# Performance work log

Hardware: AMD Instinct MI355X
Metric: run time of the kernel (lower is better)

## Reference

```python
import math
import jax, jax.numpy as jnp
import numpy as np

_INIT_LOG_GAIN = math.log(5.0)
B, L, D = 4, 1024, 256


def setup_inputs() -> dict:
    key = jax.random.key(0)
    kq, kk = jax.random.split(key)
    q = jax.random.normal(kq, (B, L, D), dtype=jnp.float32)
    k = jax.random.normal(kk, (B, L, D), dtype=jnp.float32)
    P_prev = jnp.zeros((B, D, D), dtype=jnp.float32)
    log_gain = jnp.full((D,), _INIT_LOG_GAIN, dtype=jnp.float32)
    output_scale = jnp.ones((D,), dtype=jnp.float32)
    return {"q": q, "k": k, "P_prev": P_prev, "log_gain": log_gain,
            "output_scale": output_scale}


def reference(q, k, P_prev, log_gain, output_scale):
    """Sequential rank-1 projection-state update + normalized matvec + gated tanh.

    q, k: [B, L, D]; P_prev: [B, D, D]. Returns (q_out [B,L,D], P_final [B,D,D]).
    """
    gain = jnp.exp(log_gain)  # effective gain, [D]

    def step(P, qk_t):
        q_t, k_t = qk_t                                   # each [B, D]
        P = P + jnp.einsum('bi,bj->bij', k_t, k_t)        # rank-1 update
        fro = jnp.sqrt(jnp.sum(P * P, axis=(-2, -1), keepdims=True))
        P_norm = P / (fro + 1e-7)
        q_aligned = jnp.einsum('bij,bj->bi', P_norm, q_t)
        q_safe = jnp.tanh(gain * q_aligned) * output_scale
        return P, q_safe

    # scan over the L time axis
    P_final, outs = jax.lax.scan(step, P_prev,
                                 (jnp.swapaxes(q, 0, 1), jnp.swapaxes(k, 0, 1)))
    q_out = jnp.swapaxes(outs, 0, 1)  # [B, L, D]
    return q_out, P_final
```

## Files before the change

### kernel.cpp

```cpp
#include <hip/hip_runtime.h>
#include <math.h>


typedef __attribute__((ext_vector_type(8))) short bf16x8;
typedef __attribute__((ext_vector_type(4))) float f32x4;

__device__ __forceinline__ unsigned short f2bf(float x) {
    union { float f; unsigned u; } c; c.f = x;
    return (unsigned short)((c.u + (0x7fffu + ((c.u >> 16) & 1u))) >> 16);
}
__device__ __forceinline__ unsigned f2bf2(float a, float b) {
    union { float f; unsigned u; } ca, cb; ca.f = a; cb.f = b;
    unsigned ua = ca.u + (0x7fffu + ((ca.u >> 16) & 1u));
    unsigned ub = cb.u + (0x7fffu + ((cb.u >> 16) & 1u));
    return (ua >> 16) | (ub & 0xffff0000u);
}
__device__ __forceinline__ float bf2f(unsigned short h) {
    union { unsigned u; float f; } c; c.u = ((unsigned)h) << 16; return c.f;
}
__device__ __forceinline__ void gload16(const void* g, const void* l) {
    __builtin_amdgcn_global_load_lds(
        (const __attribute__((address_space(1))) unsigned int*)g,
        (__attribute__((address_space(3))) unsigned int*)l, 16, 0, 0);
}
__device__ __forceinline__ bf16x8 ldsfrag(const unsigned short* lds, int row0, int g0, int lane) {
    int r = row0 + (lane & 15);
    int g = g0 + (lane >> 4);
    return *(const bf16x8*)(lds + r * 64 + (((g ^ (r & 7)) & 7) << 3));
}
#define MFMA16(a, b, c) __builtin_amdgcn_mfma_f32_16x16x32_bf16(a, b, c, 0, 0, 0)

__global__ __launch_bounds__(256) void k_prep(
    const float* __restrict__ Q, const float* __restrict__ K,
    const float* __restrict__ Pprev,
    unsigned short* __restrict__ Qb, unsigned short* __restrict__ Kb,
    unsigned short* __restrict__ KThi, unsigned short* __restrict__ KTlo,
    float* __restrict__ basePart, int B_, int L, int D)
{
    __shared__ float lds[64 * 65];
    int tid = threadIdx.x, lane = tid & 63, w = tid >> 6;
    int nDt = D >> 6, nLt = L >> 6;
    int nC = B_ * nLt * nDt;
    int id = blockIdx.x;
    if (id < nC) {
        int dt = id % nDt, lt = (id / nDt) % nLt, b = id / (nDt * nLt);
        int l0 = lt * 64, d0 = dt * 64;
        const float* Qf = Q + (size_t)b * L * D;
        const float* Kf = K + (size_t)b * L * D;
        unsigned short* Qbp = Qb + (size_t)b * L * D;
        unsigned short* Kbp = Kb + (size_t)b * L * D;
        unsigned short* KThp = KThi + (size_t)b * D * L;
        unsigned short* KTlp = KTlo + (size_t)b * D * L;
        int r = tid >> 2, cq = (tid & 3) << 4;
#pragma unroll
        for (int i = 0; i < 16; i += 4) {
            float4 qv = *(const float4*)(Qf + (size_t)(l0 + r) * D + d0 + cq + i);
            float4 kv = *(const float4*)(Kf + (size_t)(l0 + r) * D + d0 + cq + i);
            uint2 qo; qo.x = f2bf2(qv.x, qv.y); qo.y = f2bf2(qv.z, qv.w);
            uint2 ko; ko.x = f2bf2(kv.x, kv.y); ko.y = f2bf2(kv.z, kv.w);
            *(uint2*)(Qbp + (size_t)(l0 + r) * D + d0 + cq + i) = qo;
            *(uint2*)(Kbp + (size_t)(l0 + r) * D + d0 + cq + i) = ko;
            lds[r * 65 + cq + i]     = kv.x; lds[r * 65 + cq + i + 1] = kv.y;
            lds[r * 65 + cq + i + 2] = kv.z; lds[r * 65 + cq + i + 3] = kv.w;
        }
        __syncthreads();
        int d2 = tid >> 2, cl = (tid & 3) << 4;
#pragma unroll
        for (int i = 0; i < 16; i += 2) {
            float v0 = lds[(cl + i) * 65 + d2];
            float v1 = lds[(cl + i + 1) * 65 + d2];
            unsigned short h0 = f2bf(v0), h1 = f2bf(v1);
            size_t off = (size_t)(d0 + d2) * L + l0 + cl + i;
            *(unsigned*)(KThp + off) = (unsigned)h0 | ((unsigned)h1 << 16);
            *(unsigned*)(KTlp + off) = f2bf2(v0 - bf2f(h0), v1 - bf2f(h1));
        }
    } else {
        int id2 = id - nC;
        int n = D * D / 16;
        const float* P = Pprev + (size_t)(id2 >> 4) * D * D + (size_t)(id2 & 15) * n;
        float s = 0.f;
        for (int i = tid * 4; i < n; i += 1024) {
            float4 vv = *(const float4*)(P + i);
            s += vv.x * vv.x + vv.y * vv.y + vv.z * vv.z + vv.w * vv.w;
        }
#pragma unroll
        for (int off = 32; off; off >>= 1) s += __shfl_down(s, off);
        if (lane == 0) lds[w] = s;
        __syncthreads();
        if (tid == 0) basePart[id2] = lds[0] + lds[1] + lds[2] + lds[3];
    }
}

__global__ __launch_bounds__(256) void k_gs(
    const unsigned short* __restrict__ Qb, const unsigned short* __restrict__ Kb,
    unsigned short* __restrict__ Sc, float* __restrict__ r2d,
    int B_, int L, int D, int nT, int nPairs)
{
    __shared__ unsigned short smem[24576];
    int tid = threadIdx.x, lane = tid & 63, w = tid >> 6;
    int fr = lane & 15, fq = lane >> 4;
    int nGS = B_ * nPairs;
    int bx = blockIdx.x;
    int id = (bx & 7) * (nGS >> 3) + (bx >> 3);

    int p = id % nPairs;
    int b = id / nPairs;
    int ti = (int)((sqrtf(8.f * p + 1.f) - 1.f) * 0.5f);
    while ((ti + 1) * (ti + 2) / 2 <= p) ti++;
    while (ti * (ti + 1) / 2 > p) ti--;
    int sj = p - ti * (ti + 1) / 2;

    const unsigned short* Qp = Qb + (size_t)b * L * D;
    const unsigned short* Kp = Kb + (size_t)b * L * D;
    int t0 = ti * 64, s0 = sj * 64;
    int wr = w >> 1, wc = w & 1;

    f32x4 g00 = {0,0,0,0}, g01 = {0,0,0,0}, g10 = {0,0,0,0}, g11 = {0,0,0,0};
    f32x4 s00 = {0,0,0,0}, s01 = {0,0,0,0}, s10 = {0,0,0,0}, s11 = {0,0,0,0};

    auto STAGE = [&](int ck, int bo) {
        const unsigned short* Kt = Kp + (size_t)t0 * D + ck * 64;
        const unsigned short* Qt = Qp + (size_t)t0 * D + ck * 64;
        const unsigned short* Ks = Kp + (size_t)s0 * D + ck * 64;
        for (int c = w; c < 8; c += 4) {
            int lrow = c * 8 + (lane >> 3);
            int gof = lrow * D + ((((lane & 7) ^ (lrow & 7)) & 7) << 3);
            gload16(Kt + gof, smem + bo + c * 512);
            gload16(Qt + gof, smem + bo + 4096 + c * 512);
            gload16(Ks + gof, smem + bo + 8192 + c * 512);
        }
    };

    STAGE(0, 0);
    __syncthreads();
    for (int ck = 0; ck < 4; ck++) {
        int cur = (ck & 1) * 12288;
        if (ck < 3) STAGE(ck + 1, 12288 - cur);
        const unsigned short* Kt = smem + cur;
        const unsigned short* Qt = Kt + 4096;
        const unsigned short* Ks = Kt + 8192;
#pragma unroll
        for (int kc = 0; kc < 2; kc++) {
            bf16x8 bK0 = ldsfrag(Ks, wc * 32, kc * 4, lane);
            bf16x8 bK1 = ldsfrag(Ks, wc * 32 + 16, kc * 4, lane);
            bf16x8 aK0 = ldsfrag(Kt, wr * 32, kc * 4, lane);
            bf16x8 aK1 = ldsfrag(Kt, wr * 32 + 16, kc * 4, lane);
            bf16x8 aQ0 = ldsfrag(Qt, wr * 32, kc * 4, lane);
            bf16x8 aQ1 = ldsfrag(Qt, wr * 32 + 16, kc * 4, lane);
            g00 = MFMA16(aK0, bK0, g00);
            g01 = MFMA16(aK0, bK1, g01);
            g10 = MFMA16(aK1, bK0, g10);
            g11 = MFMA16(aK1, bK1, g11);
            s00 = MFMA16(aQ0, bK0, s00);
            s01 = MFMA16(aQ0, bK1, s01);
            s10 = MFMA16(aQ1, bK0, s10);
            s11 = MFMA16(aQ1, bK1, s11);
        }
        __syncthreads();
    }

    float rsv[2][4] = {{0, 0, 0, 0}, {0, 0, 0, 0}};
#define EPI(MI, NI, AG, AS) { _Pragma("unroll") \
    for (int reg = 0; reg < 4; reg++) { \
        int tl = wr * 32 + MI * 16 + fq * 4 + reg; \
        int sl2 = wc * 32 + NI * 16 + fr; \
        int t = ti * 64 + tl, s = sj * 64 + sl2; \
        float g = AG[reg]; \
        float wgt = (s < t) ? 2.f : (s == t ? 1.f : 0.f); \
        rsv[MI][reg] += wgt * g * g; \
        smem[tl * 64 + sl2] = f2bf((s <= t) ? AS[reg] : 0.f); \
    } }
    EPI(0, 0, g00, s00) EPI(0, 1, g01, s01)
    EPI(1, 0, g10, s10) EPI(1, 1, g11, s11)
#undef EPI
    __syncthreads();
    {
        unsigned short* ScT = Sc + ((size_t)(b * nPairs + p) << 12);
        const uint4* s4 = (const uint4*)smem;
        uint4* d4 = (uint4*)ScT;
        d4[tid] = s4[tid];
        d4[tid + 256] = s4[tid + 256];
    }
#pragma unroll
    for (int off = 1; off < 16; off <<= 1) {
#pragma unroll
        for (int mi = 0; mi < 2; mi++)
#pragma unroll
            for (int reg = 0; reg < 4; reg++)
                rsv[mi][reg] += __shfl_xor(rsv[mi][reg], off);
    }
    if (fr == 0) {
#pragma unroll
        for (int mi = 0; mi < 2; mi++)
#pragma unroll
            for (int reg = 0; reg < 4; reg++) {
                int t = ti * 64 + wr * 32 + mi * 16 + fq * 4 + reg;
                r2d[((size_t)(b * 2 * nT) + sj * 2 + wc) * L + t] = rsv[mi][reg];
            }
    }
}

__global__ __launch_bounds__(256) void k_scan(
    const float* __restrict__ K, const float* __restrict__ Pprev,
    const float* __restrict__ r2d, const float* __restrict__ basePart,
    float* __restrict__ invfro, int B_, int L, int D, int nT)
{
    __shared__ float wred[4];
    int b = blockIdx.x;
    int tid = threadIdx.x, lane = tid & 63, w = tid >> 6;
    float bb = 0.f;
#pragma unroll
    for (int i = 0; i < 16; i++) bb += basePart[b * 16 + i];

    int t0v = tid * 4;
    int ns = 2 * ((t0v >> 6) + 1);
    float4 vs = {0.f, 0.f, 0.f, 0.f};
    for (int j = 0; j < ns; j++) {
        float4 rr = *(const float4*)&r2d[((size_t)(b * 2 * nT) + j) * L + t0v];
        vs.x += rr.x; vs.y += rr.y; vs.z += rr.z; vs.w += rr.w;
    }
    float v[4] = {vs.x, vs.y, vs.z, vs.w};
    if (bb != 0.f) {
#pragma unroll
        for (int u2 = 0; u2 < 4; u2++) {
            int t = t0v + u2;
            const float* kt = K + ((size_t)b * L + t) * D;
            const float* P = Pprev + (size_t)b * D * D;
            float c = 0.f;
            for (int i = 0; i < D; i++) {
                float a2 = 0.f;
                for (int j2 = 0; j2 < D; j2++) a2 += P[i * D + j2] * kt[j2];
                c += kt[i] * a2;
            }
            v[u2] += 2.f * c;
        }
    }
    v[1] += v[0]; v[2] += v[1]; v[3] += v[2];
    float tot = v[3], sc2 = tot;
    for (int off = 1; off < 64; off <<= 1) {
        float n2 = __shfl_up(sc2, off);
        if (lane >= off) sc2 += n2;
    }
    if (lane == 63) wred[w] = sc2;
    __syncthreads();
    float woff = 0.f;
    for (int i2 = 0; i2 < w; i2++) woff += wred[i2];
    float exc = woff + sc2 - tot;
#pragma unroll
    for (int u2 = 0; u2 < 4; u2++)
        invfro[(size_t)b * L + t0v + u2] = 1.f / (sqrtf(bb + exc + v[u2]) + 1e-7f);
}

__global__ __launch_bounds__(256) void k_yp(
    const float* __restrict__ Q,
    const float* __restrict__ Pprev, const float* __restrict__ log_gain,
    const float* __restrict__ oscale,
    const unsigned short* __restrict__ Sc, const float* __restrict__ invfro,
    const unsigned short* __restrict__ KThi, const unsigned short* __restrict__ KTlo,
    const float* __restrict__ basePart,
    float* __restrict__ out, float* __restrict__ outP,
    int B_, int L, int D, int nT, int nPairs)
{
    __shared__ unsigned short ys[18432];
    __shared__ float invf[1024];
    int tid = threadIdx.x, lane = tid & 63, w = tid >> 6;
    int fr = lane & 15, fq = lane >> 4;
    int nDh = 16;
    int nY = B_ * (nT >> 1) * nDh;
    int bx = blockIdx.x;
    int id = (bx < nY) ? ((bx & 7) * (nY >> 3) + (bx >> 3)) : bx;

    if (id < nY) {
        int dh = id % nDh;
        int u = (id / nDh) % (nT >> 1);
        int b = id / (nDh * (nT >> 1));
        int d0 = dh * 16;

        float bb = 0.f;
#pragma unroll
        for (int i = 0; i < 16; i++) bb += basePart[b * 16 + i];
        *(float4*)&invf[tid * 4] = *(const float4*)&invfro[(size_t)b * L + tid * 4];
        __syncthreads();

        int twl = w << 4;
        int ti0 = u, ti1 = nT - 1 - u;
        int pb0 = ti0 * (ti0 + 1) / 2, pb1 = ti1 * (ti1 + 1) / 2;
        const unsigned short* ScB = Sc + ((size_t)b * nPairs << 12);
        const unsigned short* KTb = KThi + (size_t)b * D * L;

        f32x4 c0 = {0, 0, 0, 0};
        f32x4 c1 = {0, 0, 0, 0};

        auto STAGE = [&](int sj, int bo) {
            const unsigned short* T1p = ScB + ((size_t)(pb1 + sj) << 12);
            if (sj <= u) {
                const unsigned short* T0p = ScB + ((size_t)(pb0 + sj) << 12);
                for (int c = w; c < 8; c += 4) {
                    int lrow = c * 8 + (lane >> 3);
                    int go = lrow * 64 + ((((lane & 7) ^ (lrow & 7)) & 7) << 3);
                    gload16(T0p + go, ys + bo + c * 512);
                }
            }
            for (int c = w; c < 8; c += 4) {
                int lrow = c * 8 + (lane >> 3);
                int go = lrow * 64 + ((((lane & 7) ^ (lrow & 7)) & 7) << 3);
                gload16(T1p + go, ys + bo + 4096 + c * 512);
            }
            if (w < 2) {
                int lrow = w * 8 + (lane >> 3);
                int gsw = (((lane & 7) ^ (lrow & 7)) & 7) << 3;
                gload16(KTb + (size_t)(d0 + lrow) * L + sj * 64 + gsw,
                        ys + bo + 8192 + w * 512);
            }
        };

        STAGE(0, 0);
        __syncthreads();
        for (int sj = 0; sj <= ti1; sj++) {
            int cur = (sj & 1) * 9216;
            if (sj < ti1) STAGE(sj + 1, 9216 - cur);
            const unsigned short* S0 = ys + cur;
            const unsigned short* S1 = S0 + 4096;
            const unsigned short* KTl = S0 + 8192;
#pragma unroll
            for (int kc = 0; kc < 2; kc++) {
                bf16x8 b0 = ldsfrag(KTl, 0, kc * 4, lane);
                bf16x8 A1 = ldsfrag(S1, twl, kc * 4, lane);
                c1 = MFMA16(A1, b0, c1);
                if (sj <= ti0) {
                    bf16x8 A0 = ldsfrag(S0, twl, kc * 4, lane);
                    c0 = MFMA16(A0, b0, c0);
                }
            }
            __syncthreads();
        }

        if (bb != 0.f) {
            const float* Qf = Q + (size_t)b * L * D;
            const float* Pb = Pprev + (size_t)b * D * D;
            for (int jj = 0; jj < D; jj++) {
                float p0 = Pb[(size_t)(d0 + fr) * D + jj];
#pragma unroll
                for (int reg = 0; reg < 4; reg++) {
                    float q0v = Qf[(size_t)(ti0 * 64 + twl + fq * 4 + reg) * D + jj];
                    float q1v = Qf[(size_t)(ti1 * 64 + twl + fq * 4 + reg) * D + jj];
                    c0[reg] += q0v * p0;
                    c1[reg] += q1v * p0;
                }
            }
        }

        float gg0 = expf(log_gain[d0 + fr]), os0 = oscale[d0 + fr];
        float* outb = out + (size_t)b * L * D;
#pragma unroll
        for (int reg = 0; reg < 4; reg++) {
            int t0 = ti0 * 64 + twl + fq * 4 + reg;
            int t1 = ti1 * 64 + twl + fq * 4 + reg;
            outb[(size_t)t0 * D + d0 + fr] = tanhf(gg0 * c0[reg] * invf[t0]) * os0;
            outb[(size_t)t1 * D + d0 + fr] = tanhf(gg0 * c1[reg] * invf[t1]) * os0;
        }
    } else {
        int id2 = id - nY;
        int b = id2 >> 4, ij = id2 & 15;
        int i0 = (ij >> 2) << 6, j0 = (ij & 3) << 6;
        const unsigned short* Hb = KThi + (size_t)b * D * L;
        const unsigned short* Lb = KTlo + (size_t)b * D * L;
        int wr = w >> 1, wc = w & 1;
        unsigned short* Ah = ys;
        unsigned short* Al = ys + 4096;
        unsigned short* Bh = ys + 8192;
        unsigned short* Bl = ys + 12288;

        f32x4 c00 = {0,0,0,0}, c01 = {0,0,0,0}, c10 = {0,0,0,0}, c11 = {0,0,0,0};
        for (int ck = 0; ck < 16; ck++) {
            __syncthreads();
            for (int c = w; c < 8; c += 4) {
                int lrow = c * 8 + (lane >> 3);
                int gof = (((lane & 7) ^ (lrow & 7)) & 7) << 3;
                gload16(Hb + (size_t)(i0 + lrow) * L + ck * 64 + gof, Ah + c * 512);
                gload16(Lb + (size_t)(i0 + lrow) * L + ck * 64 + gof, Al + c * 512);
                gload16(Hb + (size_t)(j0 + lrow) * L + ck * 64 + gof, Bh + c * 512);
                gload16(Lb + (size_t)(j0 + lrow) * L + ck * 64 + gof, Bl + c * 512);
            }
            __syncthreads();
#pragma unroll
            for (int kc = 0; kc < 2; kc++) {
                bf16x8 ah0 = ldsfrag(Ah, wr * 32, kc * 4, lane);
                bf16x8 ah1 = ldsfrag(Ah, wr * 32 + 16, kc * 4, lane);
                bf16x8 al0 = ldsfrag(Al, wr * 32, kc * 4, lane);
                bf16x8 al1 = ldsfrag(Al, wr * 32 + 16, kc * 4, lane);
                bf16x8 bh0 = ldsfrag(Bh, wc * 32, kc * 4, lane);
                bf16x8 bh1 = ldsfrag(Bh, wc * 32 + 16, kc * 4, lane);
                bf16x8 bl0 = ldsfrag(Bl, wc * 32, kc * 4, lane);
                bf16x8 bl1 = ldsfrag(Bl, wc * 32 + 16, kc * 4, lane);
                c00 = MFMA16(ah0, bh0, c00); c00 = MFMA16(ah0, bl0, c00); c00 = MFMA16(al0, bh0, c00);
                c01 = MFMA16(ah0, bh1, c01); c01 = MFMA16(ah0, bl1, c01); c01 = MFMA16(al0, bh1, c01);
                c10 = MFMA16(ah1, bh0, c10); c10 = MFMA16(ah1, bl0, c10); c10 = MFMA16(al1, bh0, c10);
                c11 = MFMA16(ah1, bh1, c11); c11 = MFMA16(ah1, bl1, c11); c11 = MFMA16(al1, bh1, c11);
            }
        }
        const float* Pb = Pprev + (size_t)b * D * D;
        float* Ob = outP + (size_t)b * D * D;
#define PEPI(MI, NI, ACC) { _Pragma("unroll") \
        for (int reg = 0; reg < 4; reg++) { \
            int i = i0 + wr * 32 + MI * 16 + fq * 4 + reg; \
            int j = j0 + wc * 32 + NI * 16 + fr; \
            Ob[(size_t)i * D + j] = Pb[(size_t)i * D + j] + ACC[reg]; \
        } }
        PEPI(0, 0, c00) PEPI(0, 1, c01) PEPI(1, 0, c10) PEPI(1, 1, c11)
#undef PEPI
    }
}

extern "C" void kernel_launch(void* const* d_in, const int* in_sizes, int n_in,
                              void* d_out, int out_size, void* d_ws, size_t ws_size,
                              hipStream_t stream) {
    const float* q = (const float*)d_in[0];
    const float* k = (const float*)d_in[1];
    const float* Pprev = (const float*)d_in[2];
    const float* log_gain = (const float*)d_in[3];
    const float* oscale = (const float*)d_in[4];

    int D = in_sizes[3];
    int B = in_sizes[2] / (D * D);
    int L = in_sizes[0] / (B * D);
    int nT = L / 64;
    int nPairs = nT * (nT + 1) / 2;
    int nDt = D >> 6;
    int nLt = L >> 6;

    if (D != 256 || L != 1024) return;

    float* out = (float*)d_out;
    float* outP = out + (size_t)B * L * D;

    size_t sR = (size_t)B * L * 2 * nT;
    size_t sBP = 64;
    size_t sI = (size_t)B * L;
    size_t sSc = (size_t)B * nPairs * 4096;
    size_t sLD = (size_t)B * L * D;
    size_t sKT = (size_t)B * D * L;
    size_t need = (sR + sBP + sI) * sizeof(float) + (sSc + 2 * sLD + 2 * sKT) * 2;
    if (ws_size < need) return;

    float* r2d = (float*)d_ws;
    float* basePart = r2d + sR;
    float* invfro = basePart + sBP;
    unsigned short* Sc = (unsigned short*)(invfro + sI);
    unsigned short* Qb = Sc + sSc;
    unsigned short* Kb = Qb + sLD;
    unsigned short* KThi = Kb + sLD;
    unsigned short* KTlo = KThi + sKT;

    int grid0 = B * nLt * nDt + B * 16;
    int grid1 = B * nPairs;
    int grid2 = B * (nT >> 1) * 16 + B * nDt * nDt;

    k_prep<<<grid0, 256, 0, stream>>>(q, k, Pprev, Qb, Kb, KThi, KTlo, basePart, B, L, D);
    k_gs<<<grid1, 256, 0, stream>>>(Qb, Kb, Sc, r2d, B, L, D, nT, nPairs);
    k_scan<<<B, 256, 0, stream>>>(k, Pprev, r2d, basePart, invfro, B, L, D, nT);
    k_yp<<<grid2, 256, 0, stream>>>(q, Pprev, log_gain, oscale, Sc, invfro, KThi, KTlo,
                                    basePart, out, outP, B, L, D, nT, nPairs);
}
```

Measured before the change: 48.86 us.

## Fold norm scan into output kernel and move P-final GEMM into Gram kernel

Removes the separate single-block-per-batch k_scan launch. Each output block now recomputes the Frobenius-norm prefix scan into shared memory from r2d, so the invfro workspace goes away. The P_final update blocks move from the output kernel into the Gram/score kernel's grid so they run alongside it. This cuts one launch and its serialization bubble, at the cost of every k_y block redundantly redoing the small 1024-element scan.

```diff
diff --git a/kernel.cpp b/kernel.cpp
--- a/kernel.cpp
+++ b/kernel.cpp
@@ -93,7 +93,9 @@
 
 __global__ __launch_bounds__(256) void k_gs(
     const unsigned short* __restrict__ Qb, const unsigned short* __restrict__ Kb,
-    unsigned short* __restrict__ Sc, float* __restrict__ r2d,
+    const unsigned short* __restrict__ KThi, const unsigned short* __restrict__ KTlo,
+    const float* __restrict__ Pprev,
+    unsigned short* __restrict__ Sc, float* __restrict__ r2d, float* __restrict__ outP,
     int B_, int L, int D, int nT, int nPairs)
 {
     __shared__ unsigned short smem[24576];
@@ -101,275 +103,114 @@
     int fr = lane & 15, fq = lane >> 4;
     int nGS = B_ * nPairs;
     int bx = blockIdx.x;
-    int id = (bx & 7) * (nGS >> 3) + (bx >> 3);
-
-    int p = id % nPairs;
-    int b = id / nPairs;
-    int ti = (int)((sqrtf(8.f * p + 1.f) - 1.f) * 0.5f);
-    while ((ti + 1) * (ti + 2) / 2 <= p) ti++;
-    while (ti * (ti + 1) / 2 > p) ti--;
-    int sj = p - ti * (ti + 1) / 2;
-
-    const unsigned short* Qp = Qb + (size_t)b * L * D;
-    const unsigned short* Kp = Kb + (size_t)b * L * D;
-    int t0 = ti * 64, s0 = sj * 64;
+    int id = (bx < nGS) ? ((bx & 7) * (nGS >> 3) + (bx >> 3)) : bx;
     int wr = w >> 1, wc = w & 1;
 
-    f32x4 g00 = {0,0,0,0}, g01 = {0,0,0,0}, g10 = {0,0,0,0}, g11 = {0,0,0,0};
-    f32x4 s00 = {0,0,0,0}, s01 = {0,0,0,0}, s10 = {0,0,0,0}, s11 = {0,0,0,0};
-
-    auto STAGE = [&](int ck, int bo) {
-        const unsigned short* Kt = Kp + (size_t)t0 * D + ck * 64;
-        const unsigned short* Qt = Qp + (size_t)t0 * D + ck * 64;
-        const unsigned short* Ks = Kp + (size_t)s0 * D + ck * 64;
-        for (int c = w; c < 8; c += 4) {
-            int lrow = c * 8 + (lane >> 3);
-            int gof = lrow * D + ((((lane & 7) ^ (lrow & 7)) & 7) << 3);
-            gload16(Kt + gof, smem + bo + c * 512);
-            gload16(Qt + gof, smem + bo + 4096 + c * 512);
-            gload16(Ks + gof, smem + bo + 8192 + c * 512);
-        }
-    };
-
-    STAGE(0, 0);
-    __syncthreads();
-    for (int ck = 0; ck < 4; ck++) {
-        int cur = (ck & 1) * 12288;
-        if (ck < 3) STAGE(ck + 1, 12288 - cur);
-        const unsigned short* Kt = smem + cur;
-        const unsigned short* Qt = Kt + 4096;
-        const unsigned short* Ks = Kt + 8192;
-#pragma unroll
-        for (int kc = 0; kc < 2; kc++) {
-            bf16x8 bK0 = ldsfrag(Ks, wc * 32, kc * 4, lane);
-            bf16x8 bK1 = ldsfrag(Ks, wc * 32 + 16, kc * 4, lane);
-            bf16x8 aK0 = ldsfrag(Kt, wr * 32, kc * 4, lane);
-            bf16x8 aK1 = ldsfrag(Kt, wr * 32 + 16, kc * 4, lane);
-            bf16x8 aQ0 = ldsfrag(Qt, wr * 32, kc * 4, lane);
-            bf16x8 aQ1 = ldsfrag(Qt, wr * 32 + 16, kc * 4, lane);
-            g00 = MFMA16(aK0, bK0, g00);
-            g01 = MFMA16(aK0, bK1, g01);
-            g10 = MFMA16(aK1, bK0, g10);
-            g11 = MFMA16(aK1, bK1, g11);
-            s00 = MFMA16(aQ0, bK0, s00);
-            s01 = MFMA16(aQ0, bK1, s01);
-            s10 = MFMA16(aQ1, bK0, s10);
-            s11 = MFMA16(aQ1, bK1, s11);
-        }
-        __syncthreads();
-    }
-
-    float rsv[2][4] = {{0, 0, 0, 0}, {0, 0, 0, 0}};
-#define EPI(MI, NI, AG, AS) { _Pragma("unroll") \
-    for (int reg = 0; reg < 4; reg++) { \
-        int tl = wr * 32 + MI * 16 + fq * 4 + reg; \
-        int sl2 = wc * 32 + NI * 16 + fr; \
-        int t = ti * 64 + tl, s = sj * 64 + sl2; \
-        float g = AG[reg]; \
-        float wgt = (s < t) ? 2.f : (s == t ? 1.f : 0.f); \
-        rsv[MI][reg] += wgt * g * g; \
-        smem[tl * 64 + sl2] = f2bf((s <= t) ? AS[reg] : 0.f); \
-    } }
-    EPI(0, 0, g00, s00) EPI(0, 1, g01, s01)
-    EPI(1, 0, g10, s10) EPI(1, 1, g11, s11)
-#undef EPI
-    __syncthreads();
-    {
-        unsigned short* ScT = Sc + ((size_t)(b * nPairs + p) << 12);
-        const uint4* s4 = (const uint4*)smem;
-        uint4* d4 = (uint4*)ScT;
-        d4[tid] = s4[tid];
-        d4[tid + 256] = s4[tid + 256];
-    }
-#pragma unroll
-    for (int off = 1; off < 16; off <<= 1) {
-#pragma unroll
-        for (int mi = 0; mi < 2; mi++)
-#pragma unroll
-            for (int reg = 0; reg < 4; reg++)
-                rsv[mi][reg] += __shfl_xor(rsv[mi][reg], off);
-    }
-    if (fr == 0) {
-#pragma unroll
-        for (int mi = 0; mi < 2; mi++)
-#pragma unroll
-            for (int reg = 0; reg < 4; reg++) {
-                int t = ti * 64 + wr * 32 + mi * 16 + fq * 4 + reg;
-                r2d[((size_t)(b * 2 * nT) + sj * 2 + wc) * L + t] = rsv[mi][reg];
-            }
-    }
-}
-
-__global__ __launch_bounds__(256) void k_scan(
-    const float* __restrict__ K, const float* __restrict__ Pprev,
-    const float* __restrict__ r2d, const float* __restrict__ basePart,
-    float* __restrict__ invfro, int B_, int L, int D, int nT)
-{
-    __shared__ float wred[4];
-    int b = blockIdx.x;
-    int tid = threadIdx.x, lane = tid & 63, w = tid >> 6;
-    float bb = 0.f;
-#pragma unroll
-    for (int i = 0; i < 16; i++) bb += basePart[b * 16 + i];
-
-    int t0v = tid * 4;
-    int ns = 2 * ((t0v >> 6) + 1);
-    float4 vs = {0.f, 0.f, 0.f, 0.f};
-    for (int j = 0; j < ns; j++) {
-        float4 rr = *(const float4*)&r2d[((size_t)(b * 2 * nT) + j) * L + t0v];
-        vs.x += rr.x; vs.y += rr.y; vs.z += rr.z; vs.w += rr.w;
-    }
-    float v[4] = {vs.x, vs.y, vs.z, vs.w};
-    if (bb != 0.f) {
-#pragma unroll
-        for (int u2 = 0; u2 < 4; u2++) {
-            int t = t0v + u2;
-            const float* kt = K + ((size_t)b * L + t) * D;
-            const float* P = Pprev + (size_t)b * D * D;
-            float c = 0.f;
-            for (int i = 0; i < D; i++) {
-                float a2 = 0.f;
-                for (int j2 = 0; j2 < D; j2++) a2 += P[i * D + j2] * kt[j2];
-                c += kt[i] * a2;
-            }
-            v[u2] += 2.f * c;
-        }
-    }
-    v[1] += v[0]; v[2] += v[1]; v[3] += v[2];
-    float tot = v[3], sc2 = tot;
-    for (int off = 1; off < 64; off <<= 1) {
-        float n2 = __shfl_up(sc2, off);
-        if (lane >= off) sc2 += n2;
-    }
-    if (lane == 63) wred[w] = sc2;
-    __syncthreads();
-    float woff = 0.f;
-    for (int i2 = 0; i2 < w; i2++) woff += wred[i2];
-    float exc = woff + sc2 - tot;
-#pragma unroll
-    for (int u2 = 0; u2 < 4; u2++)
-        invfro[(size_t)b * L + t0v + u2] = 1.f / (sqrtf(bb + exc + v[u2]) + 1e-7f);
-}
-
-__global__ __launch_bounds__(256) void k_yp(
-    const float* __restrict__ Q,
-    const float* __restrict__ Pprev, const float* __restrict__ log_gain,
-    const float* __restrict__ oscale,
-    const unsigned short* __restrict__ Sc, const float* __restrict__ invfro,
-    const unsigned short* __restrict__ KThi, const unsigned short* __restrict__ KTlo,
-    const float* __restrict__ basePart,
-    float* __restrict__ out, float* __restrict__ outP,
-    int B_, int L, int D, int nT, int nPairs)
-{
-    __shared__ unsigned short ys[18432];
-    __shared__ float invf[1024];
-    int tid = threadIdx.x, lane = tid & 63, w = tid >> 6;
-    int fr = lane & 15, fq = lane >> 4;
-    int nDh = 16;
-    int nY = B_ * (nT >> 1) * nDh;
-    int bx = blockIdx.x;
-    int id = (bx < nY) ? ((bx & 7) * (nY >> 3) + (bx >> 3)) : bx;
-
-    if (id < nY) {
-        int dh = id % nDh;
-        int u = (id / nDh) % (nT >> 1);
-        int b = id / (nDh * (nT >> 1));
-        int d0 = dh * 16;
-
-        float bb = 0.f;
-#pragma unroll
-        for (int i = 0; i < 16; i++) bb += basePart[b * 16 + i];
-        *(float4*)&invf[tid * 4] = *(const float4*)&invfro[(size_t)b * L + tid * 4];
-        __syncthreads();
-
-        int twl = w << 4;
-        int ti0 = u, ti1 = nT - 1 - u;
-        int pb0 = ti0 * (ti0 + 1) / 2, pb1 = ti1 * (ti1 + 1) / 2;
-        const unsigned short* ScB = Sc + ((size_t)b * nPairs << 12);
-        const unsigned short* KTb = KThi + (size_t)b * D * L;
-
-        f32x4 c0 = {0, 0, 0, 0};
-        f32x4 c1 = {0, 0, 0, 0};
-
-        auto STAGE = [&](int sj, int bo) {
-            const unsigned short* T1p = ScB + ((size_t)(pb1 + sj) << 12);
-            if (sj <= u) {
-                const unsigned short* T0p = ScB + ((size_t)(pb0 + sj) << 12);
-                for (int c = w; c < 8; c += 4) {
-                    int lrow = c * 8 + (lane >> 3);
-                    int go = lrow * 64 + ((((lane & 7) ^ (lrow & 7)) & 7) << 3);
-                    gload16(T0p + go, ys + bo + c * 512);
-                }
-            }
+    if (id < nGS) {
+        int p = id % nPairs;
+        int b = id / nPairs;
+        int ti = (int)((sqrtf(8.f * p + 1.f) - 1.f) * 0.5f);
+        while ((ti + 1) * (ti + 2) / 2 <= p) ti++;
+        while (ti * (ti + 1) / 2 > p) ti--;
+        int sj = p - ti * (ti + 1) / 2;
+
+        const unsigned short* Qp = Qb + (size_t)b * L * D;
+        const unsigned short* Kp = Kb + (size_t)b * L * D;
+        int t0 = ti * 64, s0 = sj * 64;
+
+        f32x4 g00 = {0,0,0,0}, g01 = {0,0,0,0}, g10 = {0,0,0,0}, g11 = {0,0,0,0};
+        f32x4 s00 = {0,0,0,0}, s01 = {0,0,0,0}, s10 = {0,0,0,0}, s11 = {0,0,0,0};
+
+        auto STAGE = [&](int ck, int bo) {
+            const unsigned short* Kt = Kp + (size_t)t0 * D + ck * 64;
+            const unsigned short* Qt = Qp + (size_t)t0 * D + ck * 64;
+            const unsigned short* Ks = Kp + (size_t)s0 * D + ck * 64;
             for (int c = w; c < 8; c += 4) {
                 int lrow = c * 8 + (lane >> 3);
-                int go = lrow * 64 + ((((lane & 7) ^ (lrow & 7)) & 7) << 3);
-                gload16(T1p + go, ys + bo + 4096 + c * 512);
-            }
-            if (w < 2) {
-                int lrow = w * 8 + (lane >> 3);
-                int gsw = (((lane & 7) ^ (lrow & 7)) & 7) << 3;
-                gload16(KTb + (size_t)(d0 + lrow) * L + sj * 64 + gsw,
-                        ys + bo + 8192 + w * 512);
+                int gof = lrow * D + ((((lane & 7) ^ (lrow & 7)) & 7) << 3);
+                gload16(Kt + gof, smem + bo + c * 512);
+                gload16(Qt + gof, smem + bo + 4096 + c * 512);
+                gload16(Ks + gof, smem + bo + 8192 + c * 512);
             }
         };
 
         STAGE(0, 0);
         __syncthreads();
-        for (int sj = 0; sj <= ti1; sj++) {
-            int cur = (sj & 1) * 9216;
-            if (sj < ti1) STAGE(sj + 1, 9216 - cur);
-            const unsigned short* S0 = ys + cur;
-            const unsigned short* S1 = S0 + 4096;
-            const unsigned short* KTl = S0 + 8192;
+        for (int ck = 0; ck < 4; ck++) {
+            int cur = (ck & 1) * 12288;
+            if (ck < 3) STAGE(ck + 1, 12288 - cur);
+            const unsigned short* Kt = smem + cur;
+            const unsigned short* Qt = Kt + 4096;
+            const unsigned short* Ks = Kt + 8192;
 #pragma unroll
             for (int kc = 0; kc < 2; kc++) {
-                bf16x8 b0 = ldsfrag(KTl, 0, kc * 4, lane);
-                bf16x8 A1 = ldsfrag(S1, twl, kc * 4, lane);
-                c1 = MFMA16(A1, b0, c1);
-                if (sj <= ti0) {
-                    bf16x8 A0 = ldsfrag(S0, twl, kc * 4, lane);
-                    c0 = MFMA16(A0, b0, c0);
+                bf16x8 bK0 = ldsfrag(Ks, wc * 32, kc * 4, lane);
+                bf16x8 bK1 = ldsfrag(Ks, wc * 32 + 16, kc * 4, lane);
+                bf16x8 aK0 = ldsfrag(Kt, wr * 32, kc * 4, lane);
+                bf16x8 aK1 = ldsfrag(Kt, wr * 32 + 16, kc * 4, lane);
+                bf16x8 aQ0 = ldsfrag(Qt, wr * 32, kc * 4, lane);
+                bf16x8 aQ1 = ldsfrag(Qt, wr * 32 + 16, kc * 4, lane);
+                g00 = MFMA16(aK0, bK0, g00);
+                g01 = MFMA16(aK0, bK1, g01);
+                g10 = MFMA16(aK1, bK0, g10);
+                g11 = MFMA16(aK1, bK1, g11);
+                s00 = MFMA16(aQ0, bK0, s00);
+                s01 = MFMA16(aQ0, bK1, s01);
+                s10 = MFMA16(aQ1, bK0, s10);
+                s11 = MFMA16(aQ1, bK1, s11);
+            }
+            __syncthreads();
+        }
+
+        float rsv[2][4] = {{0, 0, 0, 0}, {0, 0, 0, 0}};
+#define EPI(MI, NI, AG, AS) { _Pragma("unroll") \
+        for (int reg = 0; reg < 4; reg++) { \
+            int tl = wr * 32 + MI * 16 + fq * 4 + reg; \
+            int sl2 = wc * 32 + NI * 16 + fr; \
+            int t = ti * 64 + tl, s = sj * 64 + sl2; \
+            float g = AG[reg]; \
+            float wgt = (s < t) ? 2.f : (s == t ? 1.f : 0.f); \
+            rsv[MI][reg] += wgt * g * g; \
+            smem[tl * 64 + sl2] = f2bf((s <= t) ? AS[reg] : 0.f); \
+        } }
+        EPI(0, 0, g00, s00) EPI(0, 1, g01, s01)
+        EPI(1, 0, g10, s10) EPI(1, 1, g11, s11)
+#undef EPI
+        __syncthreads();
+        {
+            unsigned short* ScT = Sc + ((size_t)(b * nPairs + p) << 12);
+            const uint4* s4 = (const uint4*)smem;
+            uint4* d4 = (uint4*)ScT;
+            d4[tid] = s4[tid];
+            d4[tid + 256] = s4[tid + 256];
+        }
+#pragma unroll
+        for (int off = 1; off < 16; off <<= 1) {
+#pragma unroll
+            for (int mi = 0; mi < 2; mi++)
+#pragma unroll
+                for (int reg = 0; reg < 4; reg++)
+                    rsv[mi][reg] += __shfl_xor(rsv[mi][reg], off);
+        }
+        if (fr == 0) {
+#pragma unroll
+            for (int mi = 0; mi < 2; mi++)
+#pragma unroll
+                for (int reg = 0; reg < 4; reg++) {
+                    int t = ti * 64 + wr * 32 + mi * 16 + fq * 4 + reg;
+                    r2d[((size_t)(b * 2 * nT) + sj * 2 + wc) * L + t] = rsv[mi][reg];
                 }
-            }
-            __syncthreads();
-        }
-
-        if (bb != 0.f) {
-            const float* Qf = Q + (size_t)b * L * D;
-            const float* Pb = Pprev + (size_t)b * D * D;
-            for (int jj = 0; jj < D; jj++) {
-                float p0 = Pb[(size_t)(d0 + fr) * D + jj];
-#pragma unroll
-                for (int reg = 0; reg < 4; reg++) {
-                    float q0v = Qf[(size_t)(ti0 * 64 + twl + fq * 4 + reg) * D + jj];
-                    float q1v = Qf[(size_t)(ti1 * 64 + twl + fq * 4 + reg) * D + jj];
-                    c0[reg] += q0v * p0;
-                    c1[reg] += q1v * p0;
-                }
-            }
-        }
-
-        float gg0 = expf(log_gain[d0 + fr]), os0 = oscale[d0 + fr];
-        float* outb = out + (size_t)b * L * D;
-#pragma unroll
-        for (int reg = 0; reg < 4; reg++) {
-            int t0 = ti0 * 64 + twl + fq * 4 + reg;
-            int t1 = ti1 * 64 + twl + fq * 4 + reg;
-            outb[(size_t)t0 * D + d0 + fr] = tanhf(gg0 * c0[reg] * invf[t0]) * os0;
-            outb[(size_t)t1 * D + d0 + fr] = tanhf(gg0 * c1[reg] * invf[t1]) * os0;
         }
     } else {
-        int id2 = id - nY;
+        int id2 = id - nGS;
         int b = id2 >> 4, ij = id2 & 15;
         int i0 = (ij >> 2) << 6, j0 = (ij & 3) << 6;
         const unsigned short* Hb = KThi + (size_t)b * D * L;
         const unsigned short* Lb = KTlo + (size_t)b * D * L;
-        int wr = w >> 1, wc = w & 1;
-        unsigned short* Ah = ys;
-        unsigned short* Al = ys + 4096;
-        unsigned short* Bh = ys + 8192;
-        unsigned short* Bl = ys + 12288;
+        unsigned short* Ah = smem;
+        unsigned short* Al = smem + 4096;
+        unsigned short* Bh = smem + 8192;
+        unsigned short* Bl = smem + 12288;
 
         f32x4 c00 = {0,0,0,0}, c01 = {0,0,0,0}, c10 = {0,0,0,0}, c11 = {0,0,0,0};
         for (int ck = 0; ck < 16; ck++) {
@@ -412,6 +253,154 @@
     }
 }
 
+__global__ __launch_bounds__(256) void k_y(
+    const float* __restrict__ Q, const float* __restrict__ K,
+    const float* __restrict__ Pprev, const float* __restrict__ log_gain,
+    const float* __restrict__ oscale,
+    const unsigned short* __restrict__ Sc, const float* __restrict__ r2d,
+    const unsigned short* __restrict__ KThi, const float* __restrict__ basePart,
+    float* __restrict__ out,
+    int B_, int L, int D, int nT, int nPairs)
+{
+    __shared__ unsigned short ys[18432];
+    __shared__ float invf[1024];
+    __shared__ float wred[4];
+    int tid = threadIdx.x, lane = tid & 63, w = tid >> 6;
+    int fr = lane & 15, fq = lane >> 4;
+    int nDh = 16;
+    int nY = B_ * (nT >> 1) * nDh;
+    int bx = blockIdx.x;
+    int id = (bx & 7) * (nY >> 3) + (bx >> 3);
+
+    int dh = id % nDh;
+    int u = (id / nDh) % (nT >> 1);
+    int b = id / (nDh * (nT >> 1));
+    int d0 = dh * 16;
+
+    float bb = 0.f;
+#pragma unroll
+    for (int i = 0; i < 16; i++) bb += basePart[b * 16 + i];
+
+    {
+        int t0v = tid * 4;
+        int ns = 2 * ((t0v >> 6) + 1);
+        float4 vs = {0.f, 0.f, 0.f, 0.f};
+        for (int j = 0; j < ns; j++) {
+            float4 rr = *(const float4*)&r2d[((size_t)(b * 2 * nT) + j) * L + t0v];
+            vs.x += rr.x; vs.y += rr.y; vs.z += rr.z; vs.w += rr.w;
+        }
+        float v[4] = {vs.x, vs.y, vs.z, vs.w};
+        if (bb != 0.f) {
+#pragma unroll
+            for (int u2 = 0; u2 < 4; u2++) {
+                int t = t0v + u2;
+                const float* kt = K + ((size_t)b * L + t) * D;
+                const float* P = Pprev + (size_t)b * D * D;
+                float c = 0.f;
+                for (int i = 0; i < D; i++) {
+                    float a2 = 0.f;
+                    for (int j2 = 0; j2 < D; j2++) a2 += P[i * D + j2] * kt[j2];
+                    c += kt[i] * a2;
+                }
+                v[u2] += 2.f * c;
+            }
+        }
+        v[1] += v[0]; v[2] += v[1]; v[3] += v[2];
+        float tot = v[3], sc2 = tot;
+        for (int off = 1; off < 64; off <<= 1) {
+            float n2 = __shfl_up(sc2, off);
+            if (lane >= off) sc2 += n2;
+        }
+        if (lane == 63) wred[w] = sc2;
+        __syncthreads();
+        float woff = 0.f;
+        for (int i2 = 0; i2 < w; i2++) woff += wred[i2];
+        float exc = woff + sc2 - tot;
+#pragma unroll
+        for (int u2 = 0; u2 < 4; u2++)
+            invf[t0v + u2] = 1.f / (sqrtf(bb + exc + v[u2]) + 1e-7f);
+        __syncthreads();
+    }
+
+    int twl = w << 4;
+    int ti0 = u, ti1 = nT - 1 - u;
+    int pb0 = ti0 * (ti0 + 1) / 2, pb1 = ti1 * (ti1 + 1) / 2;
+    const unsigned short* ScB = Sc + ((size_t)b * nPairs << 12);
+    const unsigned short* KTb = KThi + (size_t)b * D * L;
+
+    f32x4 c0 = {0, 0, 0, 0};
+    f32x4 c1 = {0, 0, 0, 0};
+
+    auto STAGE = [&](int sj, int bo) {
+        const unsigned short* T1p = ScB + ((size_t)(pb1 + sj) << 12);
+        if (sj <= u) {
+            const unsigned short* T0p = ScB + ((size_t)(pb0 + sj) << 12);
+            for (int c = w; c < 8; c += 4) {
+                int lrow = c * 8 + (lane >> 3);
+                int go = lrow * 64 + ((((lane & 7) ^ (lrow & 7)) & 7) << 3);
+                gload16(T0p + go, ys + bo + c * 512);
+            }
+        }
+        for (int c = w; c < 8; c += 4) {
+            int lrow = c * 8 + (lane >> 3);
+            int go = lrow * 64 + ((((lane & 7) ^ (lrow & 7)) & 7) << 3);
+            gload16(T1p + go, ys + bo + 4096 + c * 512);
+        }
+        if (w < 2) {
+            int lrow = w * 8 + (lane >> 3);
+            int gsw = (((lane & 7) ^ (lrow & 7)) & 7) << 3;
+            gload16(KTb + (size_t)(d0 + lrow) * L + sj * 64 + gsw,
+                    ys + bo + 8192 + w * 512);
+        }
+    };
+
+    STAGE(0, 0);
+    __syncthreads();
+    for (int sj = 0; sj <= ti1; sj++) {
+        int cur = (sj & 1) * 9216;
+        if (sj < ti1) STAGE(sj + 1, 9216 - cur);
+        const unsigned short* S0 = ys + cur;
+        const unsigned short* S1 = S0 + 4096;
+        const unsigned short* KTl = S0 + 8192;
+#pragma unroll
+        for (int kc = 0; kc < 2; kc++) {
+            bf16x8 b0 = ldsfrag(KTl, 0, kc * 4, lane);
+            bf16x8 A1 = ldsfrag(S1, twl, kc * 4, lane);
+            c1 = MFMA16(A1, b0, c1);
+            if (sj <= ti0) {
+                bf16x8 A0 = ldsfrag(S0, twl, kc * 4, lane);
+                c0 = MFMA16(A0, b0, c0);
+            }
+        }
+        __syncthreads();
+    }
+
+    if (bb != 0.f) {
+        const float* Qf = Q + (size_t)b * L * D;
+        const float* Pb = Pprev + (size_t)b * D * D;
+        for (int jj = 0; jj < D; jj++) {
+            float p0 = Pb[(size_t)(d0 + fr) * D + jj];
+#pragma unroll
+            for (int reg = 0; reg < 4; reg++) {
+                float q0v = Qf[(size_t)(ti0 * 64 + twl + fq * 4 + reg) * D + jj];
+                float q1v = Qf[(size_t)(ti1 * 64 + twl + fq * 4 + reg) * D + jj];
+                c0[reg] += q0v * p0;
+                c1[reg] += q1v * p0;
+            }
+        }
+    }
+
+    float gg0 = expf(log_gain[d0 + fr]), os0 = oscale[d0 + fr];
+    float* outb = out + (size_t)b * L * D;
+#pragma unroll
+    for (int reg = 0; reg < 4; reg++) {
+        int t0 = ti0 * 64 + twl + fq * 4 + reg;
+        int t1 = ti1 * 64 + twl + fq * 4 + reg;
+        outb[(size_t)t0 * D + d0 + fr] = tanhf(gg0 * c0[reg] * invf[t0]) * os0;
+        outb[(size_t)t1 * D + d0 + fr] = tanhf(gg0 * c1[reg] * invf[t1]) * os0;
+    }
+}
+
 extern "C" void kernel_launch(void* const* d_in, const int* in_sizes, int n_in,
                               void* d_out, int out_size, void* d_ws, size_t ws_size,
                               hipStream_t stream) {
@@ -436,29 +425,27 @@
 
     size_t sR = (size_t)B * L * 2 * nT;
     size_t sBP = 64;
-    size_t sI = (size_t)B * L;
     size_t sSc = (size_t)B * nPairs * 4096;
     size_t sLD = (size_t)B * L * D;
     size_t sKT = (size_t)B * D * L;
-    size_t need = (sR + sBP + sI) * sizeof(float) + (sSc + 2 * sLD + 2 * sKT) * 2;
+    size_t need = (sR + sBP) * sizeof(float) + (sSc + 2 * sLD + 2 * sKT) * 2;
     if (ws_size < need) return;
 
     float* r2d = (float*)d_ws;
     float* basePart = r2d + sR;
-    float* invfro = basePart + sBP;
-    unsigned short* Sc = (unsigned short*)(invfro + sI);
+    unsigned short* Sc = (unsigned short*)(basePart + sBP);
     unsigned short* Qb = Sc + sSc;
     unsigned short* Kb = Qb + sLD;
     unsigned short* KThi = Kb + sLD;
     unsigned short* KTlo = KThi + sKT;
 
     int grid0 = B * nLt * nDt + B * 16;
-    int grid1 = B * nPairs;
-    int grid2 = B * (nT >> 1) * 16 + B * nDt * nDt;
+    int grid1 = B * nPairs + B * nDt * nDt;
+    int grid2 = B * (nT >> 1) * 16;
 
     k_prep<<<grid0, 256, 0, stream>>>(q, k, Pprev, Qb, Kb, KThi, KTlo, basePart, B, L, D);
-    k_gs<<<grid1, 256, 0, stream>>>(Qb, Kb, Sc, r2d, B, L, D, nT, nPairs);
-    k_scan<<<B, 256, 0, stream>>>(k, Pprev, r2d, basePart, invfro, B, L, D, nT);
-    k_yp<<<grid2, 256, 0, stream>>>(q, Pprev, log_gain, oscale, Sc, invfro, KThi, KTlo,
-                                    basePart, out, outP, B, L, D, nT, nPairs);
-}
+    k_gs<<<grid1, 256, 0, stream>>>(Qb, Kb, KThi, KTlo, Pprev, Sc, r2d, outP,
+                                    B, L, D, nT, nPairs);
+    k_y<<<grid2, 256, 0, stream>>>(q, k, Pprev, log_gain, oscale, Sc, r2d, KThi,
+                                   basePart, out, B, L, D, nT, nPairs);
+}
```

Measured after the change: 52.25 us. 1.07x slower.
